# Performance work log

Measured on AMD Instinct MI355X. Metric: run time of the kernel, lower is better.

## Reference

```python
import jax, jax.numpy as jnp
import numpy as np

B, L, D, V, K = 4, 2048, 1024, 32, 4096  # batch, seq, embedding_dim, vq_dim, num_embeddings


def setup_inputs() -> dict:
    key = jax.random.key(0)
    k0, k1, k2, k3 = jax.random.split(key, 4)
    h = jax.random.normal(k0, (B, L, D), jnp.float32)
    attn_mask = jnp.ones((B, L), jnp.float32)
    # proj: Linear(D -> V); proj_inv: Linear(V -> D)
    Wp = jax.random.normal(k1, (V, D), jnp.float32) / np.float32(np.sqrt(D))
    bp = jnp.zeros((V,), jnp.float32)
    Wpi = jax.random.normal(k2, (D, V), jnp.float32) / np.float32(np.sqrt(V))
    bpi = jnp.zeros((D,), jnp.float32)
    # embedding init uniform(-1/K, 1/K)
    emb = jax.random.uniform(k3, (K, V), jnp.float32, -1.0 / K, 1.0 / K)
    return {"h": h, "attn_mask": attn_mask, "Wp": Wp, "bp": bp,
            "Wpi": Wpi, "bpi": bpi, "emb": emb}


def reference(h, attn_mask, Wp, bp, Wpi, bpi, emb, temperature=1.0):
    # project + L2 normalize
    hp = jnp.einsum('bld,vd->blv', h, Wp) + bp            # [B,L,V]
    hp = hp / jnp.linalg.norm(hp, axis=-1, keepdims=True)
    # normalize codebook (in torch this is an in-place .data update)
    emb_n = emb / jnp.linalg.norm(emb, axis=-1, keepdims=True)  # [K,V]
    # squared euclidean distances hp vs codebook
    d = (jnp.sum(hp * hp, axis=-1, keepdims=True)
         + jnp.sum(emb_n * emb_n, axis=-1)
         - 2.0 * jnp.einsum('blv,kv->blk', hp, emb_n))    # [B,L,K]
    A = jax.nn.softmax(-d / temperature, axis=-1)         # [B,L,K]
    code = jnp.argmax(A, axis=-1)                         # [B,L]
    h_vq = jnp.einsum('blk,kv->blv', A, emb_n)            # train mode: A @ embedding
    # masked scatter into zeros is equivalent to masking out unselected positions
    m = (attn_mask == 1)
    quantized = jnp.where(m[..., None], h_vq, jnp.float32(0.0))
    vq_code = jnp.where(m, code, 0).astype(jnp.int32)
    quantized = jnp.einsum('blv,dv->bld', quantized, Wpi) + bpi
    vq_loss = jnp.float32(0.0)
    return quantized, vq_code, vq_loss
```

## Files before the change

### kernel.cpp

```cpp
#include <hip/hip_runtime.h>
#include <hip/hip_bf16.h>
#include <math.h>

#define NTOK 8192
#define DIM  1024
#define VDIM 32
#define KCODES 4096

typedef __attribute__((ext_vector_type(8))) short short8;
typedef __attribute__((ext_vector_type(4))) float f32x4;

#define MFMA16(A,B,C) __builtin_amdgcn_mfma_f32_16x16x32_bf16(A, B, C, 0, 0, 0)

__device__ __forceinline__ unsigned short f2bf(float x) {
    unsigned u = __builtin_bit_cast(unsigned, x);
    u += 0x7FFF + ((u >> 16) & 1);
    return (unsigned short)(u >> 16);
}
__device__ __forceinline__ float bf2f(unsigned short b) {
    unsigned u = ((unsigned)b) << 16;
    return __builtin_bit_cast(float, u);
}

struct U4 { unsigned x, y, z, w; };

__device__ __forceinline__ void split8(const float* p, short8* H, short8* L) {
    unsigned hh[4], ll[4];
    #pragma unroll
    for (int i = 0; i < 4; ++i) {
        unsigned short a = f2bf(p[2 * i]);
        unsigned short b = f2bf(p[2 * i + 1]);
        hh[i] = (unsigned)a | ((unsigned)b << 16);
        unsigned short la = f2bf(p[2 * i] - bf2f(a));
        unsigned short lb = f2bf(p[2 * i + 1] - bf2f(b));
        ll[i] = (unsigned)la | ((unsigned)lb << 16);
    }
    U4 uh = {hh[0], hh[1], hh[2], hh[3]};
    U4 ul = {ll[0], ll[1], ll[2], ll[3]};
    *H = __builtin_bit_cast(short8, uh);
    *L = __builtin_bit_cast(short8, ul);
}

__device__ __forceinline__ short8 pack8hi(const float* p) {
    unsigned hh[4];
    #pragma unroll
    for (int i = 0; i < 4; ++i) {
        unsigned short a = f2bf(p[2 * i]);
        unsigned short b = f2bf(p[2 * i + 1]);
        hh[i] = (unsigned)a | ((unsigned)b << 16);
    }
    U4 uh = {hh[0], hh[1], hh[2], hh[3]};
    return __builtin_bit_cast(short8, uh);
}

#define OFS_E_HI   0
#define OFS_E_LO   131072
#define OFS_ET_HI  262144
#define OFS_ET_LO  393216
#define OFS_WP_HI  524288
#define OFS_WP_LO  557056
#define OFS_WPI_HI 589824
#define OFS_WPI_LO 622592

__global__ __launch_bounds__(256) void k_prep(const float* __restrict__ emb,
                                              const float* __restrict__ Wp,
                                              const float* __restrict__ Wpi,
                                              unsigned short* __restrict__ W,
                                              float* __restrict__ loss_out) {
    __shared__ __align__(16) unsigned short Th[32][72];
    __shared__ __align__(16) unsigned short Tl[32][72];
    int bid = blockIdx.x, tid = threadIdx.x;
    if (bid < 64) {
        int cb = bid * 64;
        int c = tid >> 2, s = tid & 3;
        const float* src = emb + (size_t)(cb + c) * VDIM + s * 8;
        float4 a = *(const float4*)src;
        float4 b = *(const float4*)(src + 4);
        float ps = a.x*a.x + a.y*a.y + a.z*a.z + a.w*a.w
                 + b.x*b.x + b.y*b.y + b.z*b.z + b.w*b.w;
        ps += __shfl_xor(ps, 1);
        ps += __shfl_xor(ps, 2);
        float inv = 1.0f / sqrtf(ps);
        float vals[8] = {a.x*inv, a.y*inv, a.z*inv, a.w*inv,
                         b.x*inv, b.y*inv, b.z*inv, b.w*inv};
        short8 H, L;
        split8(vals, &H, &L);
        *(short8*)(W + OFS_E_HI + (size_t)(cb + c) * VDIM + s * 8) = H;
        *(short8*)(W + OFS_E_LO + (size_t)(cb + c) * VDIM + s * 8) = L;
        #pragma unroll
        for (int j = 0; j < 8; ++j) {
            unsigned short hb = f2bf(vals[j]);
            Th[s * 8 + j][c] = hb;
            Tl[s * 8 + j][c] = f2bf(vals[j] - bf2f(hb));
        }
        __syncthreads();
        int row = tid >> 3, seg = tid & 7;
        *(short8*)(W + OFS_ET_HI + (size_t)row * KCODES + cb + seg * 8) =
            *(const short8*)&Th[row][seg * 8];
        *(short8*)(W + OFS_ET_LO + (size_t)row * KCODES + cb + seg * 8) =
            *(const short8*)&Tl[row][seg * 8];
        if (bid == 0 && tid == 0) loss_out[0] = 0.0f;
    } else if (bid < 80) {
        int i0 = (bid - 64) * 2048 + tid * 8;
        float4 a = *(const float4*)(Wp + i0);
        float4 b = *(const float4*)(Wp + i0 + 4);
        float vals[8] = {a.x, a.y, a.z, a.w, b.x, b.y, b.z, b.w};
        short8 H, L;
        split8(vals, &H, &L);
        *(short8*)(W + OFS_WP_HI + i0) = H;
        *(short8*)(W + OFS_WP_LO + i0) = L;
    } else {
        int i0 = (bid - 80) * 2048 + tid * 8;
        float4 a = *(const float4*)(Wpi + i0);
        float4 b = *(const float4*)(Wpi + i0 + 4);
        float vals[8] = {a.x, a.y, a.z, a.w, b.x, b.y, b.z, b.w};
        short8 H, L;
        split8(vals, &H, &L);
        *(short8*)(W + OFS_WPI_HI + i0) = H;
        *(short8*)(W + OFS_WPI_LO + i0) = L;
    }
}

__global__ __launch_bounds__(512) void k_fused(const float* __restrict__ h,
                                               const float* __restrict__ mask,
                                               const unsigned short* __restrict__ W,
                                               const float* __restrict__ bp,
                                               const float* __restrict__ bpi,
                                               float* __restrict__ out,
                                               float* __restrict__ code_out) {
    __shared__ __align__(16) float red2[8][16][36];
    __shared__ __align__(16) unsigned short hpB_hi[16][40];
    __shared__ __align__(16) unsigned short hpB_lo[16][40];
    __shared__ __align__(16) unsigned short hvB_hi[16][40];
    __shared__ __align__(16) unsigned short hvB_lo[16][40];
    __shared__ float lred[8][16];
    __shared__ float amred[8][16];
    __shared__ int   aired[8][16];
    __shared__ float invl[16];

    const unsigned short* E_hi   = W + OFS_E_HI;
    const unsigned short* E_lo   = W + OFS_E_LO;
    const unsigned short* Et_hi  = W + OFS_ET_HI;
    const unsigned short* Et_lo  = W + OFS_ET_LO;
    const unsigned short* Wp_hi  = W + OFS_WP_HI;
    const unsigned short* Wp_lo  = W + OFS_WP_LO;
    const unsigned short* Wpi_hi = W + OFS_WPI_HI;
    const unsigned short* Wpi_lo = W + OFS_WPI_LO;

    int tid = threadIdx.x;
    int w = tid >> 6;
    int l = tid & 63;
    int q = l >> 4, m = l & 15;
    int tok0 = blockIdx.x * 16;
    int sig = ((m & 12) << 1) | (m & 3);
    const f32x4 zero4 = {0.f, 0.f, 0.f, 0.f};

    {
        f32x4 acc0 = zero4, acc1 = zero4;
        const float* hb = h + (size_t)(tok0 + m) * DIM + w * 128 + q * 8;
        const unsigned short* w0h = Wp_hi + (size_t)m * DIM + w * 128 + q * 8;
        const unsigned short* w0l = Wp_lo + (size_t)m * DIM + w * 128 + q * 8;
        const unsigned short* w1h = w0h + (size_t)16 * DIM;
        const unsigned short* w1l = w0l + (size_t)16 * DIM;
        #pragma unroll
        for (int c = 0; c < 4; ++c) {
            float4 a = *(const float4*)(hb + c * 32);
            float4 b = *(const float4*)(hb + c * 32 + 4);
            float va[8] = {a.x, a.y, a.z, a.w, b.x, b.y, b.z, b.w};
            short8 Bh, Bl;
            split8(va, &Bh, &Bl);
            short8 A0h = *(const short8*)(w0h + c * 32);
            short8 A0l = *(const short8*)(w0l + c * 32);
            short8 A1h = *(const short8*)(w1h + c * 32);
            short8 A1l = *(const short8*)(w1l + c * 32);
            acc0 = MFMA16(A0l, Bl, acc0); acc0 = MFMA16(A0l, Bh, acc0);
            acc0 = MFMA16(A0h, Bl, acc0); acc0 = MFMA16(A0h, Bh, acc0);
            acc1 = MFMA16(A1l, Bl, acc1); acc1 = MFMA16(A1l, Bh, acc1);
            acc1 = MFMA16(A1h, Bl, acc1); acc1 = MFMA16(A1h, Bh, acc1);
        }
        *(f32x4*)&red2[w][m][4 * q]      = acc0;
        *(f32x4*)&red2[w][m][16 + 4 * q] = acc1;
    }
    __syncthreads();
    {
        int t = tid >> 5, v = tid & 31;
        float s = bp[v];
        #pragma unroll
        for (int j = 0; j < 8; ++j) s += red2[j][t][v];
        float sq = s * s;
        #pragma unroll
        for (int off = 1; off < 32; off <<= 1) sq += __shfl_xor(sq, off);
        float nv = s * (1.0f / sqrtf(sq));
        unsigned short hb = f2bf(nv);
        hpB_hi[t][v] = hb;
        hpB_lo[t][v] = f2bf(nv - bf2f(hb));
    }
    __syncthreads();

    short8 hph = *(const short8*)&hpB_hi[m][q * 8];
    short8 hpl = *(const short8*)&hpB_lo[m][q * 8];

    f32x4 hv0 = zero4, hv1 = zero4;
    float ls = 0.f, am = -1e30f;
    int ai = 0;

    int cb = w * 512;
    size_t e0 = (size_t)(cb + sig) * VDIM + q * 8;
    size_t t0 = (size_t)sig * KCODES + cb + q * 8;
    short8 E0h = *(const short8*)(E_hi + e0);
    short8 E0l = *(const short8*)(E_lo + e0);
    short8 E1h = *(const short8*)(E_hi + e0 + 4 * VDIM);
    short8 E1l = *(const short8*)(E_lo + e0 + 4 * VDIM);
    short8 T0h = *(const short8*)(Et_hi + t0);
    short8 T0l = *(const short8*)(Et_lo + t0);
    short8 T1h = *(const short8*)(Et_hi + t0 + (size_t)4 * KCODES);
    short8 T1l = *(const short8*)(Et_lo + t0 + (size_t)4 * KCODES);

    #pragma unroll 2
    for (int c = 0; c < 16; ++c) {
        size_t ne = e0 + 1024, nt = t0 + 32;
        short8 nE0h = *(const short8*)(E_hi + ne);
        short8 nE0l = *(const short8*)(E_lo + ne);
        short8 nE1h = *(const short8*)(E_hi + ne + 4 * VDIM);
        short8 nE1l = *(const short8*)(E_lo + ne + 4 * VDIM);
        short8 nT0h = *(const short8*)(Et_hi + nt);
        short8 nT0l = *(const short8*)(Et_lo + nt);
        short8 nT1h = *(const short8*)(Et_hi + nt + (size_t)4 * KCODES);
        short8 nT1l = *(const short8*)(Et_lo + nt + (size_t)4 * KCODES);

        f32x4 s0 = MFMA16(E0l, hpl, zero4);
        s0 = MFMA16(E0l, hph, s0);
        s0 = MFMA16(E0h, hpl, s0);
        s0 = MFMA16(E0h, hph, s0);
        f32x4 s1 = MFMA16(E1l, hpl, zero4);
        s1 = MFMA16(E1l, hph, s1);
        s1 = MFMA16(E1h, hpl, s1);
        s1 = MFMA16(E1h, hph, s1);

        float p[8];
        int cbase = cb + 8 * q;
        #pragma unroll
        for (int r = 0; r < 4; ++r) {
            float sv = s0[r];
            if (sv > am) { am = sv; ai = cbase + r; }
            p[r] = __expf(2.0f * sv);
            sv = s1[r];
            if (sv > am) { am = sv; ai = cbase + 4 + r; }
            p[4 + r] = __expf(2.0f * sv);
        }
        ls += ((p[0] + p[1]) + (p[2] + p[3])) + ((p[4] + p[5]) + (p[6] + p[7]));
        short8 Ph = pack8hi(p);
        hv0 = MFMA16(T0l, Ph, hv0);
        hv0 = MFMA16(T0h, Ph, hv0);
        hv1 = MFMA16(T1l, Ph, hv1);
        hv1 = MFMA16(T1h, Ph, hv1);

        E0h = nE0h; E0l = nE0l; E1h = nE1h; E1l = nE1l;
        T0h = nT0h; T0l = nT0l; T1h = nT1h; T1l = nT1l;
        e0 = ne; t0 = nt; cb += 32;
    }

    #pragma unroll
    for (int off = 16; off <= 32; off <<= 1) {
        ls += __shfl_xor(ls, off);
        float a2 = __shfl_xor(am, off);
        int   i2 = __shfl_xor(ai, off);
        if (a2 > am || (a2 == am && i2 < ai)) { am = a2; ai = i2; }
    }
    if (q == 0) {
        lred[w][m] = ls; amred[w][m] = am; aired[w][m] = ai;
    }
    *(f32x4*)&red2[w][m][8 * q]     = hv0;
    *(f32x4*)&red2[w][m][8 * q + 4] = hv1;
    __syncthreads();

    if (tid < 16) {
        float L = 0.f, A = -1e30f;
        int I = 0x7fffffff;
        #pragma unroll
        for (int j = 0; j < 8; ++j) {
            L += lred[j][tid];
            float a2 = amred[j][tid];
            int   i2 = aired[j][tid];
            if (a2 > A || (a2 == A && i2 < I)) { A = a2; I = i2; }
        }
        bool on = (mask[tok0 + tid] == 1.0f);
        code_out[tok0 + tid] = on ? (float)I : 0.0f;
        invl[tid] = on ? (1.0f / L) : 0.0f;
    }
    float xsum;
    {
        int t = tid >> 5, v = tid & 31;
        float x = 0.f;
        #pragma unroll
        for (int j = 0; j < 8; ++j) x += red2[j][t][v];
        xsum = x;
    }
    __syncthreads();
    {
        int t = tid >> 5, v = tid & 31;
        float x = xsum * invl[t];
        unsigned short hb = f2bf(x);
        hvB_hi[t][v] = hb;
        hvB_lo[t][v] = f2bf(x - bf2f(hb));
    }
    __syncthreads();

    short8 gh = *(const short8*)&hvB_hi[m][q * 8];
    short8 gl = *(const short8*)&hvB_lo[m][q * 8];
    #pragma unroll
    for (int dt = 0; dt < 8; ++dt) {
        int dbase = w * 128 + dt * 16;
        short8 Ah = *(const short8*)(Wpi_hi + (size_t)(dbase + m) * VDIM + q * 8);
        short8 Al = *(const short8*)(Wpi_lo + (size_t)(dbase + m) * VDIM + q * 8);
        f32x4 o = MFMA16(Al, gh, zero4);
        o = MFMA16(Ah, gl, o);
        o = MFMA16(Ah, gh, o);
        float4 bias = *(const float4*)(bpi + dbase + 4 * q);
        float4 r0 = make_float4(o[0] + bias.x, o[1] + bias.y,
                                o[2] + bias.z, o[3] + bias.w);
        *(float4*)(out + (size_t)(tok0 + m) * DIM + dbase + 4 * q) = r0;
    }
}

extern "C" void kernel_launch(void* const* d_in, const int* in_sizes, int n_in,
                              void* d_out, int out_size, void* d_ws, size_t ws_size,
                              hipStream_t stream) {
    const float* h    = (const float*)d_in[0];
    const float* mask = (const float*)d_in[1];
    const float* Wp   = (const float*)d_in[2];
    const float* bp   = (const float*)d_in[3];
    const float* Wpi  = (const float*)d_in[4];
    const float* bpi  = (const float*)d_in[5];
    const float* emb  = (const float*)d_in[6];
    float* out = (float*)d_out;

    unsigned short* W = (unsigned short*)d_ws;
    float* code_out = out + (size_t)NTOK * DIM;
    float* loss_out = code_out + NTOK;

    hipLaunchKernelGGL(k_prep,  dim3(96),  dim3(256), 0, stream, emb, Wp, Wpi, W, loss_out);
    hipLaunchKernelGGL(k_fused, dim3(512), dim3(512), 0, stream, h, mask, W, bp, bpi, out, code_out);
}
```

Measured before the change: 155.0 us.

## Split fused VQ kernel into projection, split-K codebook pass, and output kernels

Replaces the single fused per-16-token kernel with three kernels. The first projects and normalises tokens into workspace, folding a log2(e)*2 scale so exp2 can be used. The second is a codebook-split VQ kernel where each block handles 64 tokens over one eighth of the codes, reusing codebook fragments across four token tiles. The third merges the partial softmax sums, argmax and weighted sums, then applies the output projection. It also drops the low-bf16 half of the transposed codebook in the A@E product and packs probabilities with a cheaper perm-based rounding, trading some precision and extra global round trips for more parallelism and codebook reuse.

```diff
diff --git a/kernel.cpp b/kernel.cpp
--- a/kernel.cpp
+++ b/kernel.cpp
@@ -7,6 +7,8 @@
 #define VDIM 32
 #define KCODES 4096
 
+#define SC 2.8853900817779268f
+
 typedef __attribute__((ext_vector_type(8))) short short8;
 typedef __attribute__((ext_vector_type(4))) float f32x4;
 
@@ -20,6 +22,13 @@
 __device__ __forceinline__ float bf2f(unsigned short b) {
     unsigned u = ((unsigned)b) << 16;
     return __builtin_bit_cast(float, u);
+}
+__device__ __forceinline__ float fexp2(float x) {
+#if __has_builtin(__builtin_amdgcn_exp2f)
+    return __builtin_amdgcn_exp2f(x);
+#else
+    return __expf(0.6931471805599453f * x);
+#endif
 }
 
 struct U4 { unsigned x, y, z, w; };
@@ -41,26 +50,33 @@
     *L = __builtin_bit_cast(short8, ul);
 }
 
-__device__ __forceinline__ short8 pack8hi(const float* p) {
-    unsigned hh[4];
-    #pragma unroll
-    for (int i = 0; i < 4; ++i) {
-        unsigned short a = f2bf(p[2 * i]);
-        unsigned short b = f2bf(p[2 * i + 1]);
-        hh[i] = (unsigned)a | ((unsigned)b << 16);
-    }
-    U4 uh = {hh[0], hh[1], hh[2], hh[3]};
+__device__ __forceinline__ short8 pack8(const float* p) {
+    unsigned u[8];
+    #pragma unroll
+    for (int j = 0; j < 8; ++j) u[j] = __builtin_bit_cast(unsigned, p[j]) + 0x8000u;
+    U4 uh;
+    uh.x = __builtin_amdgcn_perm(u[1], u[0], 0x07060302);
+    uh.y = __builtin_amdgcn_perm(u[3], u[2], 0x07060302);
+    uh.z = __builtin_amdgcn_perm(u[5], u[4], 0x07060302);
+    uh.w = __builtin_amdgcn_perm(u[7], u[6], 0x07060302);
     return __builtin_bit_cast(short8, uh);
 }
 
 #define OFS_E_HI   0
 #define OFS_E_LO   131072
 #define OFS_ET_HI  262144
-#define OFS_ET_LO  393216
-#define OFS_WP_HI  524288
-#define OFS_WP_LO  557056
-#define OFS_WPI_HI 589824
-#define OFS_WPI_LO 622592
+#define OFS_WP_HI  393216
+#define OFS_WP_LO  425984
+#define OFS_WPI_HI 458752
+#define OFS_WPI_LO 491520
+#define OFS_HP_HI  524288
+#define OFS_HP_LO  786432
+#define F32_BASE   1048576
+#define NSPLIT 8
+#define FOFS_HVP 0
+#define FOFS_LP  2097152
+#define FOFS_AMP 2162688
+#define FOFS_AIP 2228224
 
 __global__ __launch_bounds__(256) void k_prep(const float* __restrict__ emb,
                                               const float* __restrict__ Wp,
@@ -68,7 +84,6 @@
                                               unsigned short* __restrict__ W,
                                               float* __restrict__ loss_out) {
     __shared__ __align__(16) unsigned short Th[32][72];
-    __shared__ __align__(16) unsigned short Tl[32][72];
     int bid = blockIdx.x, tid = threadIdx.x;
     if (bid < 64) {
         int cb = bid * 64;
@@ -88,17 +103,11 @@
         *(short8*)(W + OFS_E_HI + (size_t)(cb + c) * VDIM + s * 8) = H;
         *(short8*)(W + OFS_E_LO + (size_t)(cb + c) * VDIM + s * 8) = L;
         #pragma unroll
-        for (int j = 0; j < 8; ++j) {
-            unsigned short hb = f2bf(vals[j]);
-            Th[s * 8 + j][c] = hb;
-            Tl[s * 8 + j][c] = f2bf(vals[j] - bf2f(hb));
-        }
+        for (int j = 0; j < 8; ++j) Th[s * 8 + j][c] = f2bf(vals[j]);
         __syncthreads();
         int row = tid >> 3, seg = tid & 7;
         *(short8*)(W + OFS_ET_HI + (size_t)row * KCODES + cb + seg * 8) =
             *(const short8*)&Th[row][seg * 8];
-        *(short8*)(W + OFS_ET_LO + (size_t)row * KCODES + cb + seg * 8) =
-            *(const short8*)&Tl[row][seg * 8];
         if (bid == 0 && tid == 0) loss_out[0] = 0.0f;
     } else if (bid < 80) {
         int i0 = (bid - 64) * 2048 + tid * 8;
@@ -121,196 +130,252 @@
     }
 }
 
-__global__ __launch_bounds__(512) void k_fused(const float* __restrict__ h,
-                                               const float* __restrict__ mask,
-                                               const unsigned short* __restrict__ W,
-                                               const float* __restrict__ bp,
-                                               const float* __restrict__ bpi,
-                                               float* __restrict__ out,
-                                               float* __restrict__ code_out) {
-    __shared__ __align__(16) float red2[8][16][36];
-    __shared__ __align__(16) unsigned short hpB_hi[16][40];
-    __shared__ __align__(16) unsigned short hpB_lo[16][40];
-    __shared__ __align__(16) unsigned short hvB_hi[16][40];
-    __shared__ __align__(16) unsigned short hvB_lo[16][40];
-    __shared__ float lred[8][16];
-    __shared__ float amred[8][16];
-    __shared__ int   aired[8][16];
+__global__ __launch_bounds__(256) void k_proj(const float* __restrict__ h,
+                                              const unsigned short* __restrict__ W,
+                                              const float* __restrict__ bp,
+                                              unsigned short* __restrict__ hp_hi,
+                                              unsigned short* __restrict__ hp_lo) {
+    __shared__ __align__(16) float red[4][16][36];
+    const unsigned short* Wp_hi = W + OFS_WP_HI;
+    const unsigned short* Wp_lo = W + OFS_WP_LO;
+    int tid = threadIdx.x;
+    int w = tid >> 6, l = tid & 63, q = l >> 4, m = l & 15;
+    int tok0 = blockIdx.x * 16;
+    const f32x4 zero4 = {0.f, 0.f, 0.f, 0.f};
+    f32x4 acc0 = zero4, acc1 = zero4;
+    const float* hb = h + (size_t)(tok0 + m) * DIM + w * 256 + q * 8;
+    const unsigned short* w0h = Wp_hi + (size_t)m * DIM + w * 256 + q * 8;
+    const unsigned short* w0l = Wp_lo + (size_t)m * DIM + w * 256 + q * 8;
+    const unsigned short* w1h = w0h + (size_t)16 * DIM;
+    const unsigned short* w1l = w0l + (size_t)16 * DIM;
+    #pragma unroll
+    for (int c = 0; c < 8; ++c) {
+        float4 a = *(const float4*)(hb + c * 32);
+        float4 b = *(const float4*)(hb + c * 32 + 4);
+        float va[8] = {a.x, a.y, a.z, a.w, b.x, b.y, b.z, b.w};
+        short8 Bh, Bl;
+        split8(va, &Bh, &Bl);
+        short8 A0h = *(const short8*)(w0h + c * 32);
+        short8 A0l = *(const short8*)(w0l + c * 32);
+        short8 A1h = *(const short8*)(w1h + c * 32);
+        short8 A1l = *(const short8*)(w1l + c * 32);
+        acc0 = MFMA16(A0l, Bl, acc0); acc0 = MFMA16(A0l, Bh, acc0);
+        acc0 = MFMA16(A0h, Bl, acc0); acc0 = MFMA16(A0h, Bh, acc0);
+        acc1 = MFMA16(A1l, Bl, acc1); acc1 = MFMA16(A1l, Bh, acc1);
+        acc1 = MFMA16(A1h, Bl, acc1); acc1 = MFMA16(A1h, Bh, acc1);
+    }
+    *(f32x4*)&red[w][m][4 * q]      = acc0;
+    *(f32x4*)&red[w][m][16 + 4 * q] = acc1;
+    __syncthreads();
+    #pragma unroll
+    for (int half = 0; half < 2; ++half) {
+        int t = (tid >> 5) + half * 8, v = tid & 31;
+        float s = bp[v];
+        #pragma unroll
+        for (int j = 0; j < 4; ++j) s += red[j][t][v];
+        float sq = s * s;
+        #pragma unroll
+        for (int off = 1; off < 32; off <<= 1) sq += __shfl_xor(sq, off);
+        float nv = s * (SC / sqrtf(sq));
+        unsigned short hb2 = f2bf(nv);
+        size_t idx = (size_t)(tok0 + t) * VDIM + v;
+        hp_hi[idx] = hb2;
+        hp_lo[idx] = f2bf(nv - bf2f(hb2));
+    }
+}
+
+__global__ __launch_bounds__(256, 4) void k_vq(const unsigned short* __restrict__ W,
+                                               float* __restrict__ hvp,
+                                               float* __restrict__ lp,
+                                               float* __restrict__ amp,
+                                               int* __restrict__ aip) {
+    __shared__ __align__(16) float red2[2][64][36];
+    __shared__ float lred[4][4][16];
+    __shared__ float amred[4][4][16];
+    __shared__ int   aired[4][4][16];
+
+    const unsigned short* E_hi  = W + OFS_E_HI;
+    const unsigned short* E_lo  = W + OFS_E_LO;
+    const unsigned short* Et_hi = W + OFS_ET_HI;
+    const unsigned short* hp_hi = W + OFS_HP_HI;
+    const unsigned short* hp_lo = W + OFS_HP_LO;
+
+    int tid = threadIdx.x;
+    int w = tid >> 6, l = tid & 63, q = l >> 4, m = l & 15;
+    int tg = blockIdx.x >> 3, sp = blockIdx.x & 7;
+    int tok0 = tg * 64;
+    int cb0 = sp * 512 + w * 128;
+    int sig = ((m & 12) << 1) | (m & 3);
+    const f32x4 zero4 = {0.f, 0.f, 0.f, 0.f};
+
+    short8 hph[4], hpl[4];
+    #pragma unroll
+    for (int t = 0; t < 4; ++t) {
+        size_t hidx = (size_t)(tok0 + t * 16 + m) * VDIM + q * 8;
+        hph[t] = *(const short8*)(hp_hi + hidx);
+        hpl[t] = *(const short8*)(hp_lo + hidx);
+    }
+
+    f32x4 hv[4][2];
+    #pragma unroll
+    for (int t = 0; t < 4; ++t) { hv[t][0] = zero4; hv[t][1] = zero4; }
+    float ls[4] = {0.f, 0.f, 0.f, 0.f};
+    float am[4] = {-1e30f, -1e30f, -1e30f, -1e30f};
+    int   ai[4] = {0, 0, 0, 0};
+
+    #pragma unroll 1
+    for (int c = 0; c < 4; ++c) {
+        int cbase = cb0 + c * 32;
+        size_t e0 = (size_t)(cbase + sig) * VDIM + q * 8;
+        short8 E0h = *(const short8*)(E_hi + e0);
+        short8 E0l = *(const short8*)(E_lo + e0);
+        short8 E1h = *(const short8*)(E_hi + e0 + 4 * VDIM);
+        short8 E1l = *(const short8*)(E_lo + e0 + 4 * VDIM);
+        size_t t0 = (size_t)sig * KCODES + cbase + q * 8;
+        short8 T0h = *(const short8*)(Et_hi + t0);
+        short8 T1h = *(const short8*)(Et_hi + t0 + (size_t)4 * KCODES);
+        int lbase = cbase + 8 * q;
+        #pragma unroll
+        for (int t = 0; t < 4; ++t) {
+            f32x4 s0 = MFMA16(E0l, hpl[t], zero4);
+            s0 = MFMA16(E0l, hph[t], s0);
+            s0 = MFMA16(E0h, hpl[t], s0);
+            s0 = MFMA16(E0h, hph[t], s0);
+            f32x4 s1 = MFMA16(E1l, hpl[t], zero4);
+            s1 = MFMA16(E1l, hph[t], s1);
+            s1 = MFMA16(E1h, hpl[t], s1);
+            s1 = MFMA16(E1h, hph[t], s1);
+            float p[8];
+            #pragma unroll
+            for (int r = 0; r < 4; ++r) {
+                float sv = s0[r];
+                if (sv > am[t]) { am[t] = sv; ai[t] = lbase + r; }
+                p[r] = fexp2(sv);
+                sv = s1[r];
+                if (sv > am[t]) { am[t] = sv; ai[t] = lbase + 4 + r; }
+                p[4 + r] = fexp2(sv);
+            }
+            ls[t] += ((p[0] + p[1]) + (p[2] + p[3])) + ((p[4] + p[5]) + (p[6] + p[7]));
+            short8 Ph = pack8(p);
+            hv[t][0] = MFMA16(T0h, Ph, hv[t][0]);
+            hv[t][1] = MFMA16(T1h, Ph, hv[t][1]);
+        }
+    }
+
+    #pragma unroll
+    for (int t = 0; t < 4; ++t) {
+        #pragma unroll
+        for (int off = 16; off <= 32; off <<= 1) {
+            ls[t] += __shfl_xor(ls[t], off);
+            float a2 = __shfl_xor(am[t], off);
+            int   i2 = __shfl_xor(ai[t], off);
+            if (a2 > am[t] || (a2 == am[t] && i2 < ai[t])) { am[t] = a2; ai[t] = i2; }
+        }
+    }
+    if (q == 0) {
+        #pragma unroll
+        for (int t = 0; t < 4; ++t) {
+            lred[w][t][m] = ls[t]; amred[w][t][m] = am[t]; aired[w][t][m] = ai[t];
+        }
+    }
+    if (w < 2) {
+        #pragma unroll
+        for (int t = 0; t < 4; ++t) {
+            *(f32x4*)&red2[w][t * 16 + m][8 * q]     = hv[t][0];
+            *(f32x4*)&red2[w][t * 16 + m][8 * q + 4] = hv[t][1];
+        }
+    }
+    __syncthreads();
+    if (w >= 2) {
+        #pragma unroll
+        for (int t = 0; t < 4; ++t) {
+            f32x4* d0 = (f32x4*)&red2[w - 2][t * 16 + m][8 * q];
+            f32x4* d1 = (f32x4*)&red2[w - 2][t * 16 + m][8 * q + 4];
+            *d0 = *d0 + hv[t][0];
+            *d1 = *d1 + hv[t][1];
+        }
+    }
+    __syncthreads();
+    if (tid < 64) {
+        int t = tid >> 4, tl = tid & 15;
+        float L = 0.f, A = -1e30f;
+        int I = 0x7fffffff;
+        #pragma unroll
+        for (int ww = 0; ww < 4; ++ww) {
+            L += lred[ww][t][tl];
+            float a2 = amred[ww][t][tl];
+            int   i2 = aired[ww][t][tl];
+            if (a2 > A || (a2 == A && i2 < I)) { A = a2; I = i2; }
+        }
+        size_t gi = (size_t)sp * NTOK + tok0 + tid;
+        lp[gi] = L; amp[gi] = A; aip[gi] = I;
+    }
+    #pragma unroll
+    for (int it = 0; it < 2; ++it) {
+        int idx = it * 256 + tid;
+        int tl = idx >> 3, v0 = (idx & 7) * 4;
+        f32x4 xs = *(const f32x4*)&red2[0][tl][v0];
+        f32x4 ys = *(const f32x4*)&red2[1][tl][v0];
+        f32x4 sum = xs + ys;
+        *(f32x4*)(hvp + ((size_t)sp * NTOK + tok0 + tl) * VDIM + v0) = sum;
+    }
+}
+
+__global__ __launch_bounds__(256) void k_out(const unsigned short* __restrict__ W,
+                                             const float* __restrict__ mask,
+                                             const float* __restrict__ bpi,
+                                             const float* __restrict__ hvp,
+                                             const float* __restrict__ lp,
+                                             const float* __restrict__ amp,
+                                             const int* __restrict__ aip,
+                                             float* __restrict__ out,
+                                             float* __restrict__ code_out) {
     __shared__ float invl[16];
-
-    const unsigned short* E_hi   = W + OFS_E_HI;
-    const unsigned short* E_lo   = W + OFS_E_LO;
-    const unsigned short* Et_hi  = W + OFS_ET_HI;
-    const unsigned short* Et_lo  = W + OFS_ET_LO;
-    const unsigned short* Wp_hi  = W + OFS_WP_HI;
-    const unsigned short* Wp_lo  = W + OFS_WP_LO;
+    __shared__ __align__(16) unsigned short hvh[16][40];
+    __shared__ __align__(16) unsigned short hvl[16][40];
     const unsigned short* Wpi_hi = W + OFS_WPI_HI;
     const unsigned short* Wpi_lo = W + OFS_WPI_LO;
-
     int tid = threadIdx.x;
-    int w = tid >> 6;
-    int l = tid & 63;
-    int q = l >> 4, m = l & 15;
     int tok0 = blockIdx.x * 16;
-    int sig = ((m & 12) << 1) | (m & 3);
     const f32x4 zero4 = {0.f, 0.f, 0.f, 0.f};
 
-    {
-        f32x4 acc0 = zero4, acc1 = zero4;
-        const float* hb = h + (size_t)(tok0 + m) * DIM + w * 128 + q * 8;
-        const unsigned short* w0h = Wp_hi + (size_t)m * DIM + w * 128 + q * 8;
-        const unsigned short* w0l = Wp_lo + (size_t)m * DIM + w * 128 + q * 8;
-        const unsigned short* w1h = w0h + (size_t)16 * DIM;
-        const unsigned short* w1l = w0l + (size_t)16 * DIM;
-        #pragma unroll
-        for (int c = 0; c < 4; ++c) {
-            float4 a = *(const float4*)(hb + c * 32);
-            float4 b = *(const float4*)(hb + c * 32 + 4);
-            float va[8] = {a.x, a.y, a.z, a.w, b.x, b.y, b.z, b.w};
-            short8 Bh, Bl;
-            split8(va, &Bh, &Bl);
-            short8 A0h = *(const short8*)(w0h + c * 32);
-            short8 A0l = *(const short8*)(w0l + c * 32);
-            short8 A1h = *(const short8*)(w1h + c * 32);
-            short8 A1l = *(const short8*)(w1l + c * 32);
-            acc0 = MFMA16(A0l, Bl, acc0); acc0 = MFMA16(A0l, Bh, acc0);
-            acc0 = MFMA16(A0h, Bl, acc0); acc0 = MFMA16(A0h, Bh, acc0);
-            acc1 = MFMA16(A1l, Bl, acc1); acc1 = MFMA16(A1l, Bh, acc1);
-            acc1 = MFMA16(A1h, Bl, acc1); acc1 = MFMA16(A1h, Bh, acc1);
-        }
-        *(f32x4*)&red2[w][m][4 * q]      = acc0;
-        *(f32x4*)&red2[w][m][16 + 4 * q] = acc1;
-    }
-    __syncthreads();
-    {
-        int t = tid >> 5, v = tid & 31;
-        float s = bp[v];
-        #pragma unroll
-        for (int j = 0; j < 8; ++j) s += red2[j][t][v];
-        float sq = s * s;
-        #pragma unroll
-        for (int off = 1; off < 32; off <<= 1) sq += __shfl_xor(sq, off);
-        float nv = s * (1.0f / sqrtf(sq));
-        unsigned short hb = f2bf(nv);
-        hpB_hi[t][v] = hb;
-        hpB_lo[t][v] = f2bf(nv - bf2f(hb));
-    }
-    __syncthreads();
-
-    short8 hph = *(const short8*)&hpB_hi[m][q * 8];
-    short8 hpl = *(const short8*)&hpB_lo[m][q * 8];
-
-    f32x4 hv0 = zero4, hv1 = zero4;
-    float ls = 0.f, am = -1e30f;
-    int ai = 0;
-
-    int cb = w * 512;
-    size_t e0 = (size_t)(cb + sig) * VDIM + q * 8;
-    size_t t0 = (size_t)sig * KCODES + cb + q * 8;
-    short8 E0h = *(const short8*)(E_hi + e0);
-    short8 E0l = *(const short8*)(E_lo + e0);
-    short8 E1h = *(const short8*)(E_hi + e0 + 4 * VDIM);
-    short8 E1l = *(const short8*)(E_lo + e0 + 4 * VDIM);
-    short8 T0h = *(const short8*)(Et_hi + t0);
-    short8 T0l = *(const short8*)(Et_lo + t0);
-    short8 T1h = *(const short8*)(Et_hi + t0 + (size_t)4 * KCODES);
-    short8 T1l = *(const short8*)(Et_lo + t0 + (size_t)4 * KCODES);
-
-    #pragma unroll 2
-    for (int c = 0; c < 16; ++c) {
-        size_t ne = e0 + 1024, nt = t0 + 32;
-        short8 nE0h = *(const short8*)(E_hi + ne);
-        short8 nE0l = *(const short8*)(E_lo + ne);
-        short8 nE1h = *(const short8*)(E_hi + ne + 4 * VDIM);
-        short8 nE1l = *(const short8*)(E_lo + ne + 4 * VDIM);
-        short8 nT0h = *(const short8*)(Et_hi + nt);
-        short8 nT0l = *(const short8*)(Et_lo + nt);
-        short8 nT1h = *(const short8*)(Et_hi + nt + (size_t)4 * KCODES);
-        short8 nT1l = *(const short8*)(Et_lo + nt + (size_t)4 * KCODES);
-
-        f32x4 s0 = MFMA16(E0l, hpl, zero4);
-        s0 = MFMA16(E0l, hph, s0);
-        s0 = MFMA16(E0h, hpl, s0);
-        s0 = MFMA16(E0h, hph, s0);
-        f32x4 s1 = MFMA16(E1l, hpl, zero4);
-        s1 = MFMA16(E1l, hph, s1);
-        s1 = MFMA16(E1h, hpl, s1);
-        s1 = MFMA16(E1h, hph, s1);
-
-        float p[8];
-        int cbase = cb + 8 * q;
-        #pragma unroll
-        for (int r = 0; r < 4; ++r) {
-            float sv = s0[r];
-            if (sv > am) { am = sv; ai = cbase + r; }
-            p[r] = __expf(2.0f * sv);
-            sv = s1[r];
-            if (sv > am) { am = sv; ai = cbase + 4 + r; }
-            p[4 + r] = __expf(2.0f * sv);
-        }
-        ls += ((p[0] + p[1]) + (p[2] + p[3])) + ((p[4] + p[5]) + (p[6] + p[7]));
-        short8 Ph = pack8hi(p);
-        hv0 = MFMA16(T0l, Ph, hv0);
-        hv0 = MFMA16(T0h, Ph, hv0);
-        hv1 = MFMA16(T1l, Ph, hv1);
-        hv1 = MFMA16(T1h, Ph, hv1);
-
-        E0h = nE0h; E0l = nE0l; E1h = nE1h; E1l = nE1l;
-        T0h = nT0h; T0l = nT0l; T1h = nT1h; T1l = nT1l;
-        e0 = ne; t0 = nt; cb += 32;
-    }
-
-    #pragma unroll
-    for (int off = 16; off <= 32; off <<= 1) {
-        ls += __shfl_xor(ls, off);
-        float a2 = __shfl_xor(am, off);
-        int   i2 = __shfl_xor(ai, off);
-        if (a2 > am || (a2 == am && i2 < ai)) { am = a2; ai = i2; }
-    }
-    if (q == 0) {
-        lred[w][m] = ls; amred[w][m] = am; aired[w][m] = ai;
-    }
-    *(f32x4*)&red2[w][m][8 * q]     = hv0;
-    *(f32x4*)&red2[w][m][8 * q + 4] = hv1;
-    __syncthreads();
-
     if (tid < 16) {
+        int tk = tok0 + tid;
         float L = 0.f, A = -1e30f;
         int I = 0x7fffffff;
         #pragma unroll
-        for (int j = 0; j < 8; ++j) {
-            L += lred[j][tid];
-            float a2 = amred[j][tid];
-            int   i2 = aired[j][tid];
+        for (int sp = 0; sp < NSPLIT; ++sp) {
+            size_t gi = (size_t)sp * NTOK + tk;
+            L += lp[gi];
+            float a2 = amp[gi];
+            int   i2 = aip[gi];
             if (a2 > A || (a2 == A && i2 < I)) { A = a2; I = i2; }
         }
-        bool on = (mask[tok0 + tid] == 1.0f);
-        code_out[tok0 + tid] = on ? (float)I : 0.0f;
+        bool on = (mask[tk] == 1.0f);
+        code_out[tk] = on ? (float)I : 0.0f;
         invl[tid] = on ? (1.0f / L) : 0.0f;
     }
-    float xsum;
-    {
-        int t = tid >> 5, v = tid & 31;
+    __syncthreads();
+    #pragma unroll
+    for (int it = 0; it < 2; ++it) {
+        int idx = it * 256 + tid;
+        int t = idx >> 5, v = idx & 31;
         float x = 0.f;
         #pragma unroll
-        for (int j = 0; j < 8; ++j) x += red2[j][t][v];
-        xsum = x;
+        for (int sp = 0; sp < NSPLIT; ++sp)
+            x += hvp[((size_t)sp * NTOK + tok0 + t) * VDIM + v];
+        x *= invl[t];
+        unsigned short hb = f2bf(x);
+        hvh[t][v] = hb;
+        hvl[t][v] = f2bf(x - bf2f(hb));
     }
     __syncthreads();
-    {
-        int t = tid >> 5, v = tid & 31;
-        float x = xsum * invl[t];
-        unsigned short hb = f2bf(x);
-        hvB_hi[t][v] = hb;
-        hvB_lo[t][v] = f2bf(x - bf2f(hb));
-    }
-    __syncthreads();
-
-    short8 gh = *(const short8*)&hvB_hi[m][q * 8];
-    short8 gl = *(const short8*)&hvB_lo[m][q * 8];
-    #pragma unroll
-    for (int dt = 0; dt < 8; ++dt) {
-        int dbase = w * 128 + dt * 16;
+    int w = tid >> 6, l = tid & 63, q = l >> 4, m = l & 15;
+    short8 gh = *(const short8*)&hvh[m][q * 8];
+    short8 gl = *(const short8*)&hvl[m][q * 8];
+    #pragma unroll
+    for (int dt = 0; dt < 16; ++dt) {
+        int dbase = w * 256 + dt * 16;
         short8 Ah = *(const short8*)(Wpi_hi + (size_t)(dbase + m) * VDIM + q * 8);
         short8 Al = *(const short8*)(Wpi_lo + (size_t)(dbase + m) * VDIM + q * 8);
         f32x4 o = MFMA16(Al, gh, zero4);
@@ -336,9 +401,19 @@
     float* out = (float*)d_out;
 
     unsigned short* W = (unsigned short*)d_ws;
+    unsigned short* hp_hi = W + OFS_HP_HI;
+    unsigned short* hp_lo = W + OFS_HP_LO;
+    float* fbase = (float*)(W + F32_BASE);
+    float* hvp = fbase + FOFS_HVP;
+    float* lpp = fbase + FOFS_LP;
+    float* ampp = fbase + FOFS_AMP;
+    int*   aipp = (int*)(fbase + FOFS_AIP);
+
     float* code_out = out + (size_t)NTOK * DIM;
     float* loss_out = code_out + NTOK;
 
-    hipLaunchKernelGGL(k_prep,  dim3(96),  dim3(256), 0, stream, emb, Wp, Wpi, W, loss_out);
-    hipLaunchKernelGGL(k_fused, dim3(512), dim3(512), 0, stream, h, mask, W, bp, bpi, out, code_out);
-}
+    hipLaunchKernelGGL(k_prep, dim3(96),   dim3(256), 0, stream, emb, Wp, Wpi, W, loss_out);
+    hipLaunchKernelGGL(k_proj, dim3(512),  dim3(256), 0, stream, h, W, bp, hp_hi, hp_lo);
+    hipLaunchKernelGGL(k_vq,   dim3(1024), dim3(256), 0, stream, W, hvp, lpp, ampp, aipp);
+    hipLaunchKernelGGL(k_out,  dim3(512),  dim3(256), 0, stream, W, mask, bpi, hvp, lpp, ampp, aipp, out, code_out);
+}
```

Result: faster. 142.8 us (-7.9%).
